# Kernel optimization log

Measured on AMD Instinct MI355X. Metric: run time of the kernel, lower is better.

The kernel has to match this reference:

```python
import jax, jax.numpy as jnp
import numpy as np

NBITS = 8
QMAX = 2 ** (NBITS - 1) - 1  # 127
EPS_S = 1e-8


def ste_round(x):
    # straight-through estimator round (matches HAWQ ste_round)
    return x + jax.lax.stop_gradient(jnp.round(x) - x)


def quant_act(x):
    # symmetric per-tensor 8-bit fake quantization (QuantAct)
    s = jnp.maximum(jnp.max(jnp.abs(x)) / QMAX, EPS_S)
    xq = jnp.clip(ste_round(x / s), -QMAX - 1, QMAX)
    return xq * s, s


def quant_weight_per_channel(w, axis=0):
    # symmetric per-output-channel 8-bit fake quantization (weights)
    red = tuple(i for i in range(w.ndim) if i != axis)
    s = jnp.maximum(jnp.max(jnp.abs(w), axis=red, keepdims=True) / QMAX, EPS_S)
    wq = jnp.clip(ste_round(w / s), -QMAX - 1, QMAX)
    return wq * s, s


def setup_inputs() -> dict:
    key = jax.random.key(0)
    ks = jax.random.split(key, 6)
    B, Cin, Cout, H, W = 32, 256, 128, 56, 56
    x = jax.random.normal(ks[0], (B, Cin, H, W), jnp.float32)
    bn_gamma = 1.0 + 0.1 * jax.random.normal(ks[1], (Cin,), jnp.float32)
    bn_beta = 0.1 * jax.random.normal(ks[2], (Cin,), jnp.float32)
    bn_mean = 0.1 * jax.random.normal(ks[3], (Cin,), jnp.float32)
    bn_var = jax.random.uniform(ks[4], (Cin,), jnp.float32, minval=0.5, maxval=1.5)
    conv_w = jax.random.normal(ks[5], (Cout, Cin), jnp.float32) * (1.0 / np.sqrt(Cin))
    return {"x": x, "bn_gamma": bn_gamma, "bn_beta": bn_beta,
            "bn_mean": bn_mean, "bn_var": bn_var, "conv_w": conv_w}


def reference(x, bn_gamma, bn_beta, bn_mean, bn_var, conv_w):
    bn_eps = 1e-5
    # --- QuantAct on incoming activations ---
    x, act_s = quant_act(x)
    # --- QuantBn: fold BN into per-channel scale/shift, quantize folded weight ---
    w_fold = bn_gamma * jax.lax.rsqrt(bn_var + bn_eps)        # [Cin]
    b_fold = bn_beta - bn_mean * w_fold                       # [Cin]
    wq, bn_s = quant_weight_per_channel(w_fold, axis=0)
    x = x * wq[None, :, None, None] + b_fold[None, :, None, None]
    # --- QuantAct1: requantize post-BN output (act_s * bn_s threaded) ---
    x, act_s = quant_act(x)
    # --- ReLU ---
    x = jax.nn.relu(x)
    # --- QuantConv2d: 1x1 conv, per-output-channel quantized weight ---
    cwq, conv_s = quant_weight_per_channel(conv_w, axis=0)    # [Cout, Cin]
    x = jnp.einsum('bchw,oc->bohw', x, cwq)                   # [B, Cout, H, W]
    # --- QuantAct2: requantize post-conv output ---
    x, act_s = quant_act(x)
    # --- QuantAveragePool2d(2,2): pool in integer domain, rescale back ---
    B, C, H, W = x.shape
    x_int = x / act_s
    pooled = x_int.reshape(B, C, H // 2, 2, W // 2, 2).mean(axis=(3, 5))
    x = pooled * act_s
    # --- QuantAct3 ---
    x, act_s = quant_act(x)
    return x, act_s
```

## Files before the change

### kernel.cpp

```cpp
#include <hip/hip_runtime.h>
#include <math.h>

#define QMAXF 127.0f
#define EPSF  1e-8f
#define CIN   256
#define COUT  128
#define HW    3136
#define W_    56
#define NPOOL 3211264
#define POOL_BLOCKS 1792

typedef unsigned short u16;
typedef unsigned int   u32;
typedef __attribute__((ext_vector_type(8))) short s16x8;
typedef __attribute__((ext_vector_type(4))) float f32x4;

#define WQ_OFF   8
#define BF_OFF   264
#define EMAX_OFF 520
#define EMIN_OFF 776
#define CS_OFF   1032
#define CWB_OFF  1160
#define Y_OFF    17544

__device__ __forceinline__ float qclip(float v) {
    return fminf(fmaxf(v, -128.0f), 127.0f);
}
__device__ __forceinline__ u16 bf16bits(float f) {
    return (u16)(__float_as_uint(f) >> 16);
}
__device__ __forceinline__ u32 encf(float f) {
    u32 u = __float_as_uint(f);
    return (u & 0x80000000u) ? ~u : (u | 0x80000000u);
}
__device__ __forceinline__ float decf(u32 k) {
    return __uint_as_float((k & 0x80000000u) ? (k ^ 0x80000000u) : ~k);
}

__device__ __forceinline__ void block_max_atomic(float v, float* red, u32* dst) {
    #pragma unroll
    for (int off = 32; off > 0; off >>= 1) v = fmaxf(v, __shfl_xor(v, off));
    const int lane = threadIdx.x & 63, wid = threadIdx.x >> 6;
    if (lane == 0) red[wid] = v;
    __syncthreads();
    if (threadIdx.x == 0) {
        const int nw = blockDim.x >> 6;
        float m = red[0];
        for (int i = 1; i < nw; ++i) m = fmaxf(m, red[i]);
        atomicMax(dst, __float_as_uint(m));
    }
}

__device__ __forceinline__ float xform(float xv, float s1, float s2,
                                       float wqc, float bfc) {
    const float q1 = qclip(rintf(xv / s1));
    const float xd = __fmul_rn(q1, s1);
    const float x2 = __fadd_rn(__fmul_rn(xd, wqc), bfc);
    const float q2 = qclip(rintf(x2 / s2));
    return fmaxf(q2, 0.0f);
}

__global__ void k0w(const float* __restrict__ cw, float* __restrict__ ws) {
    const int t = threadIdx.x;
    if (blockIdx.x == COUT) {
        ((u32*)ws)[EMAX_OFF + t] = 0u;
        ((u32*)ws)[EMIN_OFF + t] = 0xFFFFFFFFu;
        if (t < 2) ((u32*)ws)[2 + t] = 0u;
        return;
    }
    __shared__ float red[4];
    const int o = blockIdx.x;
    const float wv = cw[o * CIN + t];
    float v = fabsf(wv);
    #pragma unroll
    for (int off = 32; off > 0; off >>= 1) v = fmaxf(v, __shfl_xor(v, off));
    if ((t & 63) == 0) red[t >> 6] = v;
    __syncthreads();
    const float mx = fmaxf(fmaxf(red[0], red[1]), fmaxf(red[2], red[3]));
    const float s = fmaxf(mx / QMAXF, EPSF);
    const float q = qclip(rintf(wv / s));
    ((u16*)(ws + CWB_OFF))[o * CIN + t] = bf16bits(q);
    if (t == 0) ws[CS_OFF + o] = s;
}

__global__ void k1_minmax(const float* __restrict__ x, float* __restrict__ ws) {
    __shared__ float red[8];
    const int row = blockIdx.x;
    const float4* xr = (const float4*)(x + (size_t)row * HW);
    float mx = -3.402823466e38f, mn = 3.402823466e38f;
    for (int i = threadIdx.x; i < HW / 4; i += 256) {
        const float4 v = xr[i];
        mx = fmaxf(mx, fmaxf(fmaxf(v.x, v.y), fmaxf(v.z, v.w)));
        mn = fminf(mn, fminf(fminf(v.x, v.y), fminf(v.z, v.w)));
    }
    #pragma unroll
    for (int off = 32; off > 0; off >>= 1) {
        mx = fmaxf(mx, __shfl_xor(mx, off));
        mn = fminf(mn, __shfl_xor(mn, off));
    }
    if ((threadIdx.x & 63) == 0) {
        red[threadIdx.x >> 6] = mx;
        red[4 + (threadIdx.x >> 6)] = mn;
    }
    __syncthreads();
    if (threadIdx.x == 0) {
        mx = fmaxf(fmaxf(red[0], red[1]), fmaxf(red[2], red[3]));
        mn = fminf(fminf(red[4], red[5]), fminf(red[6], red[7]));
        const int c = row & (CIN - 1);
        atomicMax((u32*)ws + EMAX_OFF + c, encf(mx));
        atomicMin((u32*)ws + EMIN_OFF + c, encf(mn));
    }
}

__global__ void k0b(const float* __restrict__ g, const float* __restrict__ be,
                    const float* __restrict__ mnp, const float* __restrict__ vr,
                    float* __restrict__ ws) {
    __shared__ float red[4];
    __shared__ float s1sh;
    const int t = threadIdx.x;
    const float cmax = decf(((u32*)ws)[EMAX_OFF + t]);
    const float cmin = decf(((u32*)ws)[EMIN_OFF + t]);
    float v = fmaxf(fabsf(cmax), fabsf(cmin));
    #pragma unroll
    for (int off = 32; off > 0; off >>= 1) v = fmaxf(v, __shfl_xor(v, off));
    if ((t & 63) == 0) red[t >> 6] = v;
    __syncthreads();
    if (t == 0) {
        const float m1 = fmaxf(fmaxf(red[0], red[1]), fmaxf(red[2], red[3]));
        ws[0] = m1;
        s1sh = fmaxf(m1 / QMAXF, EPSF);
    }
    __syncthreads();
    const float s1 = s1sh;
    const float wf = g[t] / sqrtf(vr[t] + 1e-5f);
    const float bf = be[t] - mnp[t] * wf;
    const float sw = fmaxf(fabsf(wf) / QMAXF, EPSF);
    const float q  = qclip(rintf(wf / sw));
    const float wqd = __fmul_rn(q, sw);
    ws[WQ_OFF + t] = wqd;
    ws[BF_OFF + t] = bf;
    const float q1h = qclip(rintf(cmax / s1));
    const float q1l = qclip(rintf(cmin / s1));
    const float xh = __fadd_rn(__fmul_rn(__fmul_rn(q1h, s1), wqd), bf);
    const float xl = __fadd_rn(__fmul_rn(__fmul_rn(q1l, s1), wqd), bf);
    float m2 = fmaxf(fabsf(xh), fabsf(xl));
    __syncthreads();
    #pragma unroll
    for (int off = 32; off > 0; off >>= 1) m2 = fmaxf(m2, __shfl_xor(m2, off));
    if ((t & 63) == 0) red[t >> 6] = m2;
    __syncthreads();
    if (t == 0) ws[1] = fmaxf(fmaxf(red[0], red[1]), fmaxf(red[2], red[3]));
}

__device__ __forceinline__ void stage_store(u16* __restrict__ Xb, u16* __restrict__ Wb,
                                            const float* __restrict__ xr,
                                            const s16x8* __restrict__ wreg,
                                            int t, int ck, float s1, float s2,
                                            const float* __restrict__ Wqs,
                                            const float* __restrict__ Bfs) {
    const int p = t & 63, kh = t >> 6;
    u32 pk[8];
    #pragma unroll
    for (int j = 0; j < 8; ++j) {
        const int c0 = ck + kh * 16 + 2 * j;
        const float a0 = xform(xr[2 * j],     s1, s2, Wqs[c0],     Bfs[c0]);
        const float a1 = xform(xr[2 * j + 1], s1, s2, Wqs[c0 + 1], Bfs[c0 + 1]);
        pk[j] = (__float_as_uint(a0) >> 16) | (__float_as_uint(a1) & 0xFFFF0000u);
    }
    const int g0 = kh * 2;
    uint4 v0; v0.x = pk[0]; v0.y = pk[1]; v0.z = pk[2]; v0.w = pk[3];
    uint4 v1; v1.x = pk[4]; v1.y = pk[5]; v1.z = pk[6]; v1.w = pk[7];
    *(uint4*)&Xb[p * 64 + (((g0 + p + (p >> 3)) & 7) * 8)]     = v0;
    *(uint4*)&Xb[p * 64 + (((g0 + 1 + p + (p >> 3)) & 7) * 8)] = v1;
    #pragma unroll
    for (int ps = 0; ps < 4; ++ps) {
        const int o = ps * 32 + (t >> 3);
        *(s16x8*)&Wb[o * 64 + ((((t & 7) + o + (o >> 3)) & 7) * 8)] = wreg[ps];
    }
}

__global__ __launch_bounds__(256) void k3_mfma(const float* __restrict__ x,
                                               float* __restrict__ ws) {
    __shared__ __align__(16) u16 Xs[2][64 * 64];
    __shared__ __align__(16) u16 Wt[2][128 * 64];
    __shared__ float Wqs[CIN], Bfs[CIN], Css[COUT];
    __shared__ float red[4];

    const int t   = threadIdx.x;
    const int b   = blockIdx.x / 49;
    const int hw0 = (blockIdx.x % 49) * 64;
    const int l   = t & 63, w = t >> 6;
    const int wc  = (w >> 1) * 64;
    const int wp  = (w & 1) * 32;

    const float s1 = fmaxf(ws[0] / QMAXF, EPSF);
    const float s2 = fmaxf(ws[1] / QMAXF, EPSF);

    Wqs[t] = ws[WQ_OFF + t];
    Bfs[t] = ws[BF_OFF + t];
    if (t < COUT) Css[t] = ws[CS_OFF + t];

    const u16* cwb = (const u16*)(ws + CWB_OFF);
    const int p  = t & 63;
    const int kh = t >> 6;
    const float* xb = x + (size_t)b * CIN * HW + hw0 + p;

    float xr[16];
    s16x8 wreg[4];

    #pragma unroll
    for (int ps = 0; ps < 4; ++ps)
        wreg[ps] = *(const s16x8*)(cwb + (ps * 32 + (t >> 3)) * CIN + (t & 7) * 8);
    #pragma unroll
    for (int j = 0; j < 16; ++j)
        xr[j] = xb[(kh * 16 + j) * HW];

    f32x4 acc[4][2];
    #pragma unroll
    for (int m = 0; m < 4; ++m)
        #pragma unroll
        for (int n = 0; n < 2; ++n) acc[m][n] = (f32x4)0.0f;

    __syncthreads();
    stage_store(Xs[0], Wt[0], xr, wreg, t, 0, s1, s2, Wqs, Bfs);
    __syncthreads();

    #pragma unroll
    for (int it = 0; it < 4; ++it) {
        const int ckn = (it + 1) * 64;
        if (it < 3) {
            #pragma unroll
            for (int ps = 0; ps < 4; ++ps)
                wreg[ps] = *(const s16x8*)(cwb + (ps * 32 + (t >> 3)) * CIN + ckn + (t & 7) * 8);
            #pragma unroll
            for (int j = 0; j < 16; ++j)
                xr[j] = xb[(ckn + kh * 16 + j) * HW];
        }
        const u16* Xb = Xs[it & 1];
        const u16* Wb = Wt[it & 1];
        #pragma unroll
        for (int ks = 0; ks < 2; ++ks) {
            const int ch = ks * 4 + (l >> 4);
            s16x8 xf[2], wfr[4];
            #pragma unroll
            for (int n = 0; n < 2; ++n) {
                const int pp = wp + n * 16 + (l & 15);
                xf[n] = *(const s16x8*)&Xb[pp * 64 + (((ch + pp + (pp >> 3)) & 7) * 8)];
            }
            #pragma unroll
            for (int m = 0; m < 4; ++m) {
                const int o = wc + m * 16 + (l & 15);
                wfr[m] = *(const s16x8*)&Wb[o * 64 + (((ch + o + (o >> 3)) & 7) * 8)];
            }
            #pragma unroll
            for (int m = 0; m < 4; ++m)
                #pragma unroll
                for (int n = 0; n < 2; ++n)
                    acc[m][n] = __builtin_amdgcn_mfma_f32_16x16x32_bf16(
                                    wfr[m], xf[n], acc[m][n], 0, 0, 0);
        }
        if (it < 3)
            stage_store(Xs[(it + 1) & 1], Wt[(it + 1) & 1], xr, wreg, t, ckn,
                        s1, s2, Wqs, Bfs);
        __syncthreads();
    }

    float mloc = 0.0f;
    #pragma unroll
    for (int m = 0; m < 4; ++m) {
        #pragma unroll
        for (int n = 0; n < 2; ++n) {
            const int pix = hw0 + wp + n * 16 + (l & 15);
            #pragma unroll
            for (int r = 0; r < 4; ++r) {
                const int o = wc + m * 16 + (l >> 4) * 4 + r;
                const float sc = __fmul_rn(s2, Css[o]);
                const float val = __fmul_rn(acc[m][n][r], sc);
                ws[Y_OFF + ((size_t)(b * COUT + o)) * HW + pix] = val;
                mloc = fmaxf(mloc, fabsf(val));
            }
        }
    }
    block_max_atomic(mloc, red, (u32*)ws + 2);
}

__global__ void k4_pool(float* __restrict__ ws, float* __restrict__ out) {
    __shared__ float red[4];
    const float s3 = fmaxf(ws[2] / QMAXF, EPSF);
    float mloc = 0.0f;
    const int nq2 = NPOOL / 2;
    for (int pp = blockIdx.x * 256 + threadIdx.x; pp < nq2;
         pp += POOL_BLOCKS * 256) {
        const int j2  = pp % 14;
        const int tmp = pp / 14;
        const int i   = tmp % 28;
        const int bo  = tmp / 28;
        const float* yb = ws + Y_OFF + (size_t)bo * HW + (2 * i) * W_ + 4 * j2;
        const float4 r0 = *(const float4*)yb;
        const float4 r1 = *(const float4*)(yb + W_);
        const float q00 = qclip(rintf(r0.x / s3)), q01 = qclip(rintf(r0.y / s3));
        const float q02 = qclip(rintf(r0.z / s3)), q03 = qclip(rintf(r0.w / s3));
        const float q10 = qclip(rintf(r1.x / s3)), q11 = qclip(rintf(r1.y / s3));
        const float q12 = qclip(rintf(r1.z / s3)), q13 = qclip(rintf(r1.w / s3));
        const float p0 = __fmul_rn(__fmul_rn((q00 + q01) + (q10 + q11), 0.25f), s3);
        const float p1 = __fmul_rn(__fmul_rn((q02 + q03) + (q12 + q13), 0.25f), s3);
        float2 pv; pv.x = p0; pv.y = p1;
        *(float2*)(out + (size_t)bo * 784 + i * 28 + 2 * j2) = pv;
        mloc = fmaxf(mloc, fmaxf(fabsf(p0), fabsf(p1)));
    }
    block_max_atomic(mloc, red, (u32*)ws + 3);
}

__global__ void k5_final(float* __restrict__ out, const float* __restrict__ ws) {
    const float s4 = fmaxf(ws[3] / QMAXF, EPSF);
    const int n4 = NPOOL / 4;
    for (int i = blockIdx.x * 256 + threadIdx.x; i < n4; i += 3136 * 256) {
        float4 v = *(float4*)(out + 4 * (size_t)i);
        v.x = __fmul_rn(qclip(rintf(v.x / s4)), s4);
        v.y = __fmul_rn(qclip(rintf(v.y / s4)), s4);
        v.z = __fmul_rn(qclip(rintf(v.z / s4)), s4);
        v.w = __fmul_rn(qclip(rintf(v.w / s4)), s4);
        *(float4*)(out + 4 * (size_t)i) = v;
    }
    if (blockIdx.x == 0 && threadIdx.x == 0) out[NPOOL] = s4;
}

extern "C" void kernel_launch(void* const* d_in, const int* in_sizes, int n_in,
                              void* d_out, int out_size, void* d_ws, size_t ws_size,
                              hipStream_t stream) {
    const float* x     = (const float*)d_in[0];
    const float* gamma = (const float*)d_in[1];
    const float* beta  = (const float*)d_in[2];
    const float* mean  = (const float*)d_in[3];
    const float* var   = (const float*)d_in[4];
    const float* cw    = (const float*)d_in[5];
    float* out = (float*)d_out;
    float* ws  = (float*)d_ws;

    hipLaunchKernelGGL(k0w, dim3(COUT + 1), dim3(256), 0, stream, cw, ws);
    hipLaunchKernelGGL(k1_minmax, dim3(32 * CIN), dim3(256), 0, stream, x, ws);
    hipLaunchKernelGGL(k0b, dim3(1), dim3(256), 0, stream, gamma, beta, mean, var, ws);
    hipLaunchKernelGGL(k3_mfma, dim3(1568), dim3(256), 0, stream, x, ws);
    hipLaunchKernelGGL(k4_pool, dim3(POOL_BLOCKS), dim3(256), 0, stream, ws, out);
    hipLaunchKernelGGL(k5_final, dim3(3136), dim3(256), 0, stream, out, ws);
}
```

Before: 127.4 us.

## Replace per-element BN requant math with per-channel LUT and halve GEMM tile

Adds a small kernel that precomputes, for each input channel and each possible first-quantization level, the bf16 value after BN fold, requantization and ReLU. The GEMM staging then does one divide, a round and a LUT gather instead of two divides and the surrounding arithmetic. The GEMM tile shrinks from 64 to 32 pixels per block, which doubles the grid and drops LDS double-buffering in favour of single buffers with extra barriers. The output scale product is also precomputed. The cost is an extra launch, LUT gathers from global memory, and less overlap of loads with MFMA work.

```diff
diff --git a/kernel.cpp b/kernel.cpp
--- a/kernel.cpp
+++ b/kernel.cpp
@@ -20,8 +20,10 @@
 #define EMAX_OFF 520
 #define EMIN_OFF 776
 #define CS_OFF   1032
-#define CWB_OFF  1160
-#define Y_OFF    17544
+#define CSS2_OFF 1160
+#define CWB_OFF  1288
+#define LUT_OFF  17672
+#define Y_OFF    50440
 
 __device__ __forceinline__ float qclip(float v) {
     return fminf(fmaxf(v, -128.0f), 127.0f);
@@ -49,15 +51,6 @@
         for (int i = 1; i < nw; ++i) m = fmaxf(m, red[i]);
         atomicMax(dst, __float_as_uint(m));
     }
-}
-
-__device__ __forceinline__ float xform(float xv, float s1, float s2,
-                                       float wqc, float bfc) {
-    const float q1 = qclip(rintf(xv / s1));
-    const float xd = __fmul_rn(q1, s1);
-    const float x2 = __fadd_rn(__fmul_rn(xd, wqc), bfc);
-    const float q2 = qclip(rintf(x2 / s2));
-    return fmaxf(q2, 0.0f);
 }
 
 __global__ void k0w(const float* __restrict__ cw, float* __restrict__ ws) {
@@ -152,77 +145,88 @@
     if (t == 0) ws[1] = fmaxf(fmaxf(red[0], red[1]), fmaxf(red[2], red[3]));
 }
 
-__device__ __forceinline__ void stage_store(u16* __restrict__ Xb, u16* __restrict__ Wb,
-                                            const float* __restrict__ xr,
-                                            const s16x8* __restrict__ wreg,
-                                            int t, int ck, float s1, float s2,
-                                            const float* __restrict__ Wqs,
-                                            const float* __restrict__ Bfs) {
-    const int p = t & 63, kh = t >> 6;
-    u32 pk[8];
-    #pragma unroll
-    for (int j = 0; j < 8; ++j) {
-        const int c0 = ck + kh * 16 + 2 * j;
-        const float a0 = xform(xr[2 * j],     s1, s2, Wqs[c0],     Bfs[c0]);
-        const float a1 = xform(xr[2 * j + 1], s1, s2, Wqs[c0 + 1], Bfs[c0 + 1]);
-        pk[j] = (__float_as_uint(a0) >> 16) | (__float_as_uint(a1) & 0xFFFF0000u);
-    }
-    const int g0 = kh * 2;
-    uint4 v0; v0.x = pk[0]; v0.y = pk[1]; v0.z = pk[2]; v0.w = pk[3];
-    uint4 v1; v1.x = pk[4]; v1.y = pk[5]; v1.z = pk[6]; v1.w = pk[7];
-    *(uint4*)&Xb[p * 64 + (((g0 + p + (p >> 3)) & 7) * 8)]     = v0;
-    *(uint4*)&Xb[p * 64 + (((g0 + 1 + p + (p >> 3)) & 7) * 8)] = v1;
+__global__ void k0L(float* __restrict__ ws) {
+    const int c = blockIdx.x;
+    const int t = threadIdx.x;
+    const float s1 = fmaxf(ws[0] / QMAXF, EPSF);
+    const float s2 = fmaxf(ws[1] / QMAXF, EPSF);
+    const float wqd = ws[WQ_OFF + c];
+    const float bf  = ws[BF_OFF + c];
+    const float q1f = (float)(t - 127);
+    const float xd  = __fmul_rn(q1f, s1);
+    const float x2  = __fadd_rn(__fmul_rn(xd, wqd), bf);
+    const float q2  = qclip(rintf(x2 / s2));
+    const float a   = fmaxf(q2, 0.0f);
+    ((u16*)(ws + LUT_OFF))[(c << 8) + t] = bf16bits(a);
+    if (c == 0 && t < COUT)
+        ws[CSS2_OFF + t] = __fmul_rn(s2, ws[CS_OFF + t]);
+}
+
+__device__ __forceinline__ void stage32(u16* __restrict__ Xs, u16* __restrict__ Wt,
+                                        const float* __restrict__ xr,
+                                        const s16x8* __restrict__ wreg,
+                                        int t, int ck, float s1,
+                                        const u16* __restrict__ lut) {
+    const int p = t & 31, kh = t >> 5;
+    u32 pk[4];
+    #pragma unroll
+    for (int jj = 0; jj < 4; ++jj) {
+        const int c0 = ck + kh * 8 + 2 * jj;
+        const float q1a = rintf(xr[2 * jj] / s1);
+        const float q1b = rintf(xr[2 * jj + 1] / s1);
+        const u32 lo = lut[(c0 << 8) + 127 + (int)q1a];
+        const u32 hi = lut[((c0 + 1) << 8) + 127 + (int)q1b];
+        pk[jj] = lo | (hi << 16);
+    }
+    uint4 v; v.x = pk[0]; v.y = pk[1]; v.z = pk[2]; v.w = pk[3];
+    *(uint4*)&Xs[p * 64 + (((kh + p + (p >> 3)) & 7) * 8)] = v;
     #pragma unroll
     for (int ps = 0; ps < 4; ++ps) {
         const int o = ps * 32 + (t >> 3);
-        *(s16x8*)&Wb[o * 64 + ((((t & 7) + o + (o >> 3)) & 7) * 8)] = wreg[ps];
+        *(s16x8*)&Wt[o * 64 + ((((t & 7) + o + (o >> 3)) & 7) * 8)] = wreg[ps];
     }
 }
 
 __global__ __launch_bounds__(256) void k3_mfma(const float* __restrict__ x,
                                                float* __restrict__ ws) {
-    __shared__ __align__(16) u16 Xs[2][64 * 64];
-    __shared__ __align__(16) u16 Wt[2][128 * 64];
-    __shared__ float Wqs[CIN], Bfs[CIN], Css[COUT];
+    __shared__ __align__(16) u16 Xs[32 * 64];
+    __shared__ __align__(16) u16 Wt[128 * 64];
+    __shared__ float Css2s[COUT];
     __shared__ float red[4];
 
     const int t   = threadIdx.x;
-    const int b   = blockIdx.x / 49;
-    const int hw0 = (blockIdx.x % 49) * 64;
+    const int b   = blockIdx.x / 98;
+    const int hw0 = (blockIdx.x % 98) * 32;
     const int l   = t & 63, w = t >> 6;
-    const int wc  = (w >> 1) * 64;
-    const int wp  = (w & 1) * 32;
+    const int wc  = w * 32;
 
     const float s1 = fmaxf(ws[0] / QMAXF, EPSF);
-    const float s2 = fmaxf(ws[1] / QMAXF, EPSF);
-
-    Wqs[t] = ws[WQ_OFF + t];
-    Bfs[t] = ws[BF_OFF + t];
-    if (t < COUT) Css[t] = ws[CS_OFF + t];
-
+    const u16* lut = (const u16*)(ws + LUT_OFF);
     const u16* cwb = (const u16*)(ws + CWB_OFF);
-    const int p  = t & 63;
-    const int kh = t >> 6;
+
+    if (t < COUT) Css2s[t] = ws[CSS2_OFF + t];
+
+    const int p  = t & 31;
+    const int kh = t >> 5;
     const float* xb = x + (size_t)b * CIN * HW + hw0 + p;
 
-    float xr[16];
+    float xr[8];
     s16x8 wreg[4];
 
     #pragma unroll
     for (int ps = 0; ps < 4; ++ps)
         wreg[ps] = *(const s16x8*)(cwb + (ps * 32 + (t >> 3)) * CIN + (t & 7) * 8);
     #pragma unroll
-    for (int j = 0; j < 16; ++j)
-        xr[j] = xb[(kh * 16 + j) * HW];
-
-    f32x4 acc[4][2];
-    #pragma unroll
-    for (int m = 0; m < 4; ++m)
+    for (int j = 0; j < 8; ++j)
+        xr[j] = xb[(kh * 8 + j) * HW];
+
+    f32x4 acc[2][2];
+    #pragma unroll
+    for (int m = 0; m < 2; ++m)
         #pragma unroll
         for (int n = 0; n < 2; ++n) acc[m][n] = (f32x4)0.0f;
 
-    __syncthreads();
-    stage_store(Xs[0], Wt[0], xr, wreg, t, 0, s1, s2, Wqs, Bfs);
+    stage32(Xs, Wt, xr, wreg, t, 0, s1, lut);
     __syncthreads();
 
     #pragma unroll
@@ -233,49 +237,47 @@
             for (int ps = 0; ps < 4; ++ps)
                 wreg[ps] = *(const s16x8*)(cwb + (ps * 32 + (t >> 3)) * CIN + ckn + (t & 7) * 8);
             #pragma unroll
-            for (int j = 0; j < 16; ++j)
-                xr[j] = xb[(ckn + kh * 16 + j) * HW];
+            for (int j = 0; j < 8; ++j)
+                xr[j] = xb[(ckn + kh * 8 + j) * HW];
         }
-        const u16* Xb = Xs[it & 1];
-        const u16* Wb = Wt[it & 1];
         #pragma unroll
         for (int ks = 0; ks < 2; ++ks) {
             const int ch = ks * 4 + (l >> 4);
-            s16x8 xf[2], wfr[4];
+            s16x8 xf[2], wfr[2];
             #pragma unroll
             for (int n = 0; n < 2; ++n) {
-                const int pp = wp + n * 16 + (l & 15);
-                xf[n] = *(const s16x8*)&Xb[pp * 64 + (((ch + pp + (pp >> 3)) & 7) * 8)];
+                const int pp = n * 16 + (l & 15);
+                xf[n] = *(const s16x8*)&Xs[pp * 64 + (((ch + pp + (pp >> 3)) & 7) * 8)];
             }
             #pragma unroll
-            for (int m = 0; m < 4; ++m) {
+            for (int m = 0; m < 2; ++m) {
                 const int o = wc + m * 16 + (l & 15);
-                wfr[m] = *(const s16x8*)&Wb[o * 64 + (((ch + o + (o >> 3)) & 7) * 8)];
+                wfr[m] = *(const s16x8*)&Wt[o * 64 + (((ch + o + (o >> 3)) & 7) * 8)];
             }
             #pragma unroll
-            for (int m = 0; m < 4; ++m)
+            for (int m = 0; m < 2; ++m)
                 #pragma unroll
                 for (int n = 0; n < 2; ++n)
                     acc[m][n] = __builtin_amdgcn_mfma_f32_16x16x32_bf16(
                                     wfr[m], xf[n], acc[m][n], 0, 0, 0);
         }
-        if (it < 3)
-            stage_store(Xs[(it + 1) & 1], Wt[(it + 1) & 1], xr, wreg, t, ckn,
-                        s1, s2, Wqs, Bfs);
-        __syncthreads();
+        if (it < 3) {
+            __syncthreads();
+            stage32(Xs, Wt, xr, wreg, t, ckn, s1, lut);
+            __syncthreads();
+        }
     }
 
     float mloc = 0.0f;
     #pragma unroll
-    for (int m = 0; m < 4; ++m) {
+    for (int m = 0; m < 2; ++m) {
         #pragma unroll
         for (int n = 0; n < 2; ++n) {
-            const int pix = hw0 + wp + n * 16 + (l & 15);
+            const int pix = hw0 + n * 16 + (l & 15);
             #pragma unroll
             for (int r = 0; r < 4; ++r) {
                 const int o = wc + m * 16 + (l >> 4) * 4 + r;
-                const float sc = __fmul_rn(s2, Css[o]);
-                const float val = __fmul_rn(acc[m][n][r], sc);
+                const float val = __fmul_rn(acc[m][n][r], Css2s[o]);
                 ws[Y_OFF + ((size_t)(b * COUT + o)) * HW + pix] = val;
                 mloc = fmaxf(mloc, fabsf(val));
             }
@@ -340,7 +342,8 @@
     hipLaunchKernelGGL(k0w, dim3(COUT + 1), dim3(256), 0, stream, cw, ws);
     hipLaunchKernelGGL(k1_minmax, dim3(32 * CIN), dim3(256), 0, stream, x, ws);
     hipLaunchKernelGGL(k0b, dim3(1), dim3(256), 0, stream, gamma, beta, mean, var, ws);
-    hipLaunchKernelGGL(k3_mfma, dim3(1568), dim3(256), 0, stream, x, ws);
+    hipLaunchKernelGGL(k0L, dim3(256), dim3(256), 0, stream, ws);
+    hipLaunchKernelGGL(k3_mfma, dim3(3136), dim3(256), 0, stream, x, ws);
     hipLaunchKernelGGL(k4_pool, dim3(POOL_BLOCKS), dim3(256), 0, stream, ws, out);
     hipLaunchKernelGGL(k5_final, dim3(3136), dim3(256), 0, stream, out, ws);
 }
```

Result: faster. 119.4 us (-6.3%).
